# Performance work log

Hardware: AMD Instinct MI355X
Metric: run time of the kernel (lower is better)

## Reference

```python
import jax, jax.numpy as jnp
import numpy as np

N_QUBITS = 13
DEPTH = 4
DIM = 2 ** N_QUBITS
PI = 3.141592653589793

# qubit 0 = most significant bit of the basis-state index
_idx = np.arange(DIM)
BITS = np.stack([(_idx >> (N_QUBITS - 1 - q)) & 1 for q in range(N_QUBITS)], axis=1)  # (DIM, n)
SIGNS = jnp.asarray(1.0 - 2.0 * BITS, dtype=jnp.float32)                               # Z eigenvalues, (DIM, n)
PARITY = jnp.asarray((-1.0) ** BITS.sum(axis=1), dtype=jnp.float32)                    # <Z^{(x)n}> diagonal, (DIM,)
# CZ entangling chain (q, q+1): diagonal (-1)^{sum_q b_q b_{q+1}}
ENT = jnp.asarray((-1.0) ** (BITS[:, :-1] * BITS[:, 1:]).sum(axis=1), dtype=jnp.float32)


def fwht(psi):
    """Normalized fast Walsh-Hadamard transform (H on every qubit), psi: (B, DIM) complex."""
    B = psi.shape[0]
    for q in range(N_QUBITS):
        psi = psi.reshape(B, 2 ** q, 2, -1)
        psi = jnp.stack([psi[:, :, 0] + psi[:, :, 1], psi[:, :, 0] - psi[:, :, 1]], axis=2)
    return psi.reshape(B, DIM) * (2.0 ** (-N_QUBITS / 2))


def feature_map_state(x):
    """Havlicek ZZ feature map: psi = D(x) H^n D(x) H^n |0...0>.
    Diagonal phase per basis state b: sum_j x_j s_j(b) + sum_{j<k} (pi-x_j)(pi-x_k) s_j(b) s_k(b)."""
    a = PI - x                                              # (B, n)
    u = x @ SIGNS.T                                         # (B, DIM)
    v = a @ SIGNS.T                                         # (B, DIM)
    phi = u + 0.5 * (v * v - jnp.sum(a * a, axis=1, keepdims=True))  # pair term via (sum)^2 trick
    d = jnp.exp(1j * phi)                                   # complex64 diagonal
    psi = jnp.full((x.shape[0], DIM), DIM ** -0.5, dtype=jnp.complex64)  # H^n |0>
    psi = fwht(d * psi)
    return d * psi


def _apply_1q(psi, U, q):
    """Apply 2x2 complex gate U to qubit q (bit-sliced)."""
    B = psi.shape[0]
    psi = psi.reshape(B, 2 ** q, 2, -1)
    a0, a1 = psi[:, :, 0], psi[:, :, 1]
    out = jnp.stack([U[0, 0] * a0 + U[0, 1] * a1, U[1, 0] * a0 + U[1, 1] * a1], axis=2)
    return out.reshape(B, DIM)


def variational_apply(psi, theta):
    """(DEPTH+1) layers of per-qubit Rz(b)Ry(a), CZ-chain entanglers between layers."""
    th = theta.reshape(DEPTH + 1, N_QUBITS, 2)
    for l in range(DEPTH + 1):
        if l > 0:
            psi = psi * ENT
        for q in range(N_QUBITS):
            ca = jnp.cos(0.5 * th[l, q, 0])
            sa = jnp.sin(0.5 * th[l, q, 0])
            em = jnp.exp(-0.5j * th[l, q, 1])
            ep = jnp.exp(0.5j * th[l, q, 1])
            U = jnp.stack([jnp.stack([em * ca, -em * sa]), jnp.stack([ep * sa, ep * ca])])
            psi = _apply_1q(psi, U, q)
    return psi


def setup_inputs() -> dict:
    key = jax.random.key(0)
    k1, k2 = jax.random.split(key)
    x = jax.random.normal(k1, (512, N_QUBITS), dtype=jnp.float32)
    theta = 0.1 * jax.random.normal(k2, ((DEPTH + 1) * N_QUBITS * 2,), dtype=jnp.float32)
    bias = jnp.zeros((1,), dtype=jnp.float32)
    return {"x": x, "theta": theta, "bias": bias}


def reference(x, theta, bias):
    psi = feature_map_state(x)
    psi = variational_apply(psi, theta)
    prob = psi.real ** 2 + psi.imag ** 2              # (B, DIM)
    logit = prob @ PARITY + bias[0]                   # (B,)
    return jnp.stack([-logit, logit], axis=1)         # two-class logits
```

## Files before the change

### kernel.cpp

```cpp
#include <hip/hip_runtime.h>

#define NQ   13
#define DIM  8192
#define PI_F 3.14159265358979323846f
#define NT   256
#define NAMP 32

__device__ __forceinline__ int lslot(int i) { return i + (i >> 5); }
#define NSLOT (DIM + (DIM >> 5))

__device__ __forceinline__ void rsincos(float x, float* s, float* c) {
  const float INV2PI = 0.15915494309189535f;
  const float TWOPI  = 6.283185307179586f;
  float r = x * INV2PI;
  r -= rintf(r);
  float ang = r * TWOPI;
  *s = __sinf(ang);
  *c = __cosf(ang);
}

__device__ __forceinline__ void waveFence() {
  __builtin_amdgcn_wave_barrier();
  __threadfence_block();
  __builtin_amdgcn_wave_barrier();
}

__device__ __forceinline__ float2 f2fma(float s, float2 a, float2 b) {
  return make_float2(fmaf(s, a.x, b.x), fmaf(s, a.y, b.y));
}
__device__ __forceinline__ float2 f2add(float2 a, float2 b) {
  return make_float2(a.x + b.x, a.y + b.y);
}
__device__ __forceinline__ float2 f2sub(float2 a, float2 b) {
  return make_float2(a.x - b.x, a.y - b.y);
}
__device__ __forceinline__ float2 cphase(float2 v, float cs, float sn) {
  return make_float2(fmaf(cs, v.x, -sn * v.y), fmaf(cs, v.y, sn * v.x));
}
__device__ __forceinline__ float2 cmul(float2 a, float2 b) {
  return make_float2(fmaf(a.x, b.x, -a.y * b.y), fmaf(a.x, b.y, a.y * b.x));
}

template<int PAT>
__device__ __forceinline__ int ampIndex(int t, int j) {
  if constexpr (PAT == 0) return (t << 5) | j;
  else if constexpr (PAT == 1) return ((t >> 5) << 10) | (j << 5) | (t & 31);
  else return ((j >> 2) << 10) | (t << 2) | (j & 3);
}

template<int PAT>
__device__ __forceinline__ void buildTree(const float* __restrict__ w, float bias,
                                          int t, float* s) {
  float base = bias;
  if constexpr (PAT == 0) {
    #pragma unroll
    for (int k = 0; k < 8; k++) base += ((t >> k) & 1) ? w[5 + k] : 0.0f;
  } else if constexpr (PAT == 1) {
    #pragma unroll
    for (int k = 0; k < 5; k++) base += ((t >> k) & 1) ? w[k] : 0.0f;
    #pragma unroll
    for (int k = 0; k < 3; k++) base += ((t >> (5 + k)) & 1) ? w[10 + k] : 0.0f;
  } else {
    #pragma unroll
    for (int k = 0; k < 8; k++) base += ((t >> k) & 1) ? w[2 + k] : 0.0f;
  }
  constexpr int P[5] = { (PAT == 1) ? 5 : 0,
                         (PAT == 1) ? 6 : 1,
                         (PAT == 0) ? 2 : ((PAT == 1) ? 7 : 10),
                         (PAT == 0) ? 3 : ((PAT == 1) ? 8 : 11),
                         (PAT == 0) ? 4 : ((PAT == 1) ? 9 : 12) };
  s[0] = base;
  #pragma unroll
  for (int k = 0; k < 5; k++) {
    float wp = w[P[k]];
    #pragma unroll
    for (int m = 0; m < (1 << k); m++) s[m | (1 << k)] = s[m] + wp;
  }
}

template<int PAT>
__device__ __forceinline__ void loadAmps(const float2* __restrict__ sAmp,
                                         int t, float2* amp) {
  #pragma unroll
  for (int j = 0; j < NAMP; j++) {
    amp[j] = sAmp[lslot(ampIndex<PAT>(t, j))];
  }
}

template<int PAT>
__device__ __forceinline__ void storeAmps(float2* __restrict__ sAmp,
                                          int t, const float2* amp) {
  #pragma unroll
  for (int j = 0; j < NAMP; j++) {
    sAmp[lslot(ampIndex<PAT>(t, j))] = amp[j];
  }
}

template<int KB>
__device__ __forceinline__ void fwht_bit(float2* amp) {
  #pragma unroll
  for (int j = 0; j < NAMP; j++) if (!(j & (1 << KB))) {
    int j1 = j | (1 << KB);
    float2 a0 = amp[j], a1 = amp[j1];
    amp[j]  = f2add(a0, a1);
    amp[j1] = f2sub(a0, a1);
  }
}
__device__ __forceinline__ void fwht_all5(float2* amp) {
  fwht_bit<0>(amp); fwht_bit<1>(amp); fwht_bit<2>(amp);
  fwht_bit<3>(amp); fwht_bit<4>(amp);
}

template<int KB>
__device__ __forceinline__ void applyRy(float2* amp, float ta, float sa) {
  #pragma unroll
  for (int j = 0; j < NAMP; j++) if (!(j & (1 << KB))) {
    int j1 = j | (1 << KB);
    amp[j]  = f2fma(-ta, amp[j1], amp[j]);
    amp[j1] = f2fma( sa, amp[j],  amp[j1]);
    amp[j]  = f2fma(-ta, amp[j1], amp[j]);
  }
}

template<int PAT, bool INIT>
__device__ __forceinline__ void featureDiag(float2* amp,
                                            const float* __restrict__ wX,
                                            const float* __restrict__ wA,
                                            const float* __restrict__ cons, int t) {
  float u[NAMP], v[NAMP];
  buildTree<PAT>(wX, cons[0], t, u);
  buildTree<PAT>(wA, cons[1], t, v);
  float A2 = cons[2];
  #pragma unroll
  for (int j = 0; j < NAMP; j++) {
    float phi = u[j] + 0.5f * (v[j] * v[j] - A2);
    float sn, cs; rsincos(phi, &sn, &cs);
    if constexpr (INIT) amp[j] = make_float2(cs, sn);
    else                amp[j] = cphase(amp[j], cs, sn);
  }
}

__device__ __forceinline__ void applyDiagPT(float2* amp,
                                            const float* __restrict__ wb,
                                            const float* __restrict__ eR,
                                            const float* __restrict__ eI,
                                            float bias, int t) {
  float base = bias;
  #pragma unroll
  for (int k = 0; k < 8; k++) base += ((t >> k) & 1) ? wb[5 + k] : 0.0f;
  float2 c[NAMP];
  { float sn, cs; rsincos(base, &sn, &cs); c[0] = make_float2(cs, sn); }
  #pragma unroll
  for (int k = 0; k < 5; k++) {
    float2 e = make_float2(eR[k], eI[k]);
    #pragma unroll
    for (int m = 0; m < (1 << k); m++) c[m | (1 << k)] = cmul(c[m], e);
  }
  #pragma unroll
  for (int j = 0; j < NAMP; j++) {
    int i = ampIndex<0>(t, j);
    float sgn = (__popc(i & (i >> 1)) & 1) ? -1.0f : 1.0f;
    amp[j] = cphase(amp[j], c[j].x * sgn, c[j].y * sgn);
  }
}

__global__ __launch_bounds__(NT, 2) void qc_kernel(
    const float* __restrict__ xin,
    const float* __restrict__ thin,
    const float* __restrict__ bin,
    float* __restrict__ out) {
  __shared__ float2 sAmp[NSLOT];
  __shared__ float gTA[65], gSA[65];
  __shared__ float gBbit[65];
  __shared__ float eBr[65], eBi[65];
  __shared__ float wX[13], wA[13];
  __shared__ float cons[8];
  __shared__ float red[NT / 64];

  const int t = threadIdx.x;
  const int b = blockIdx.x;

  if (t < NQ) {
    float xq = xin[b * NQ + t];
    float aq = PI_F - xq;
    wX[12 - t] = -2.0f * xq;
    wA[12 - t] = -2.0f * aq;
  }
  if (t < 65) {
    float av = thin[2 * t];
    float bv = thin[2 * t + 1];
    float ca = cosf(0.5f * av);
    float sa = sinf(0.5f * av);
    gSA[t] = sa;
    gTA[t] = sa / (1.0f + ca);
    int l = t / NQ, q = t % NQ;
    int s = l * NQ + (12 - q);
    gBbit[s] = bv;
    eBr[s] = cosf(bv);
    eBi[s] = sinf(bv);
  }
  __syncthreads();
  if (t == 0) {
    float X = 0.f, A = 0.f, A2 = 0.f;
    for (int p = 0; p < NQ; p++) {
      float xq = -0.5f * wX[p], aq = -0.5f * wA[p];
      X += xq; A += aq; A2 += aq * aq;
    }
    cons[0] = X; cons[1] = A; cons[2] = A2;
    for (int l = 0; l < 5; l++) {
      float s = 0.f;
      for (int p = 0; p < NQ; p++) s += gBbit[l * NQ + p];
      cons[3 + l] = -0.5f * s;
    }
  }
  __syncthreads();

  float2 amp[NAMP];

  featureDiag<0, true>(amp, wX, wA, cons, t);
  fwht_all5(amp);
  storeAmps<0>(sAmp, t, amp);
  waveFence();

  loadAmps<1>(sAmp, t, amp);
  fwht_all5(amp);
  storeAmps<1>(sAmp, t, amp);
  __syncthreads();

  loadAmps<2>(sAmp, t, amp);
  fwht_bit<2>(amp); fwht_bit<3>(amp); fwht_bit<4>(amp);
  featureDiag<2, false>(amp, wX, wA, cons, t);
  storeAmps<2>(sAmp, t, amp);
  __syncthreads();

  float acc = 0.0f;
  for (int l = 0; l < 5; l++) {
    const int g = l * NQ;
    loadAmps<0>(sAmp, t, amp);
    if (l > 0) applyDiagPT(amp, gBbit + (l - 1) * NQ, eBr + (l - 1) * NQ,
                           eBi + (l - 1) * NQ, cons[3 + (l - 1)], t);
    applyRy<0>(amp, gTA[g + 12], gSA[g + 12]);
    applyRy<1>(amp, gTA[g + 11], gSA[g + 11]);
    applyRy<2>(amp, gTA[g + 10], gSA[g + 10]);
    applyRy<3>(amp, gTA[g + 9],  gSA[g + 9]);
    applyRy<4>(amp, gTA[g + 8],  gSA[g + 8]);
    storeAmps<0>(sAmp, t, amp);
    waveFence();
    loadAmps<1>(sAmp, t, amp);
    applyRy<0>(amp, gTA[g + 7], gSA[g + 7]);
    applyRy<1>(amp, gTA[g + 6], gSA[g + 6]);
    applyRy<2>(amp, gTA[g + 5], gSA[g + 5]);
    applyRy<3>(amp, gTA[g + 4], gSA[g + 4]);
    applyRy<4>(amp, gTA[g + 3], gSA[g + 3]);
    storeAmps<1>(sAmp, t, amp);
    __syncthreads();
    loadAmps<2>(sAmp, t, amp);
    applyRy<2>(amp, gTA[g + 2], gSA[g + 2]);
    applyRy<3>(amp, gTA[g + 1], gSA[g + 1]);
    applyRy<4>(amp, gTA[g + 0], gSA[g + 0]);
    if (l < 4) {
      storeAmps<2>(sAmp, t, amp);
      __syncthreads();
    } else {
      #pragma unroll
      for (int j = 0; j < NAMP; j++) {
        int i = ampIndex<2>(t, j);
        float p2 = fmaf(amp[j].x, amp[j].x, amp[j].y * amp[j].y);
        acc += (__popc(i) & 1) ? -p2 : p2;
      }
    }
  }

  #pragma unroll
  for (int off = 32; off > 0; off >>= 1) acc += __shfl_down(acc, off, 64);
  if ((t & 63) == 0) red[t >> 6] = acc;
  __syncthreads();
  if (t == 0) {
    float total = red[0] + red[1] + red[2] + red[3];
    float logit = total * (1.0f / 67108864.0f) + bin[0];
    out[b * 2 + 0] = -logit;
    out[b * 2 + 1] = logit;
  }
}

extern "C" void kernel_launch(void* const* d_in, const int* in_sizes, int n_in,
                              void* d_out, int out_size, void* d_ws, size_t ws_size,
                              hipStream_t stream) {
  const float* x  = (const float*)d_in[0];
  const float* th = (const float*)d_in[1];
  const float* bi = (const float*)d_in[2];
  float* out = (float*)d_out;
  int B = in_sizes[0] / NQ;
  qc_kernel<<<B, NT, 0, stream>>>(x, th, bi, out);
}
```

Before: 95.77 us.

## Regroup qubit passes into three stages and vectorize LDS amplitude access

Changes the LDS padding to two float2 per 32 amplitudes so pattern-0 and pattern-2 loads and stores can use float4 vector accesses. Reassigns qubits to passes: the pattern-2 pass now handles qubits 0,1,2,11,12 together with the entangling diagonal. This removes one LDS round trip and one __syncthreads per layer, and the last layer finishes in the pattern-1 pass. The goal is fewer LDS instructions and fewer block barriers, at the cost of a more intricate index mapping that could cause bank conflicts or correctness errors.

```diff
diff --git a/kernel.cpp b/kernel.cpp
--- a/kernel.cpp
+++ b/kernel.cpp
@@ -6,8 +6,8 @@
 #define NT   256
 #define NAMP 32
 
-__device__ __forceinline__ int lslot(int i) { return i + (i >> 5); }
-#define NSLOT (DIM + (DIM >> 5))
+__device__ __forceinline__ int lslot(int i) { return i + 2 * (i >> 5); }
+#define NSLOT (DIM + 2 * (DIM >> 5))
 
 __device__ __forceinline__ void rsincos(float x, float* s, float* c) {
   const float INV2PI = 0.15915494309189535f;
@@ -55,20 +55,14 @@
   if constexpr (PAT == 0) {
     #pragma unroll
     for (int k = 0; k < 8; k++) base += ((t >> k) & 1) ? w[5 + k] : 0.0f;
-  } else if constexpr (PAT == 1) {
-    #pragma unroll
-    for (int k = 0; k < 5; k++) base += ((t >> k) & 1) ? w[k] : 0.0f;
-    #pragma unroll
-    for (int k = 0; k < 3; k++) base += ((t >> (5 + k)) & 1) ? w[10 + k] : 0.0f;
   } else {
     #pragma unroll
     for (int k = 0; k < 8; k++) base += ((t >> k) & 1) ? w[2 + k] : 0.0f;
   }
-  constexpr int P[5] = { (PAT == 1) ? 5 : 0,
-                         (PAT == 1) ? 6 : 1,
-                         (PAT == 0) ? 2 : ((PAT == 1) ? 7 : 10),
-                         (PAT == 0) ? 3 : ((PAT == 1) ? 8 : 11),
-                         (PAT == 0) ? 4 : ((PAT == 1) ? 9 : 12) };
+  constexpr int P[5] = { 0, 1,
+                         (PAT == 0) ? 2 : 10,
+                         (PAT == 0) ? 3 : 11,
+                         (PAT == 0) ? 4 : 12 };
   s[0] = base;
   #pragma unroll
   for (int k = 0; k < 5; k++) {
@@ -78,21 +72,56 @@
   }
 }
 
-template<int PAT>
-__device__ __forceinline__ void loadAmps(const float2* __restrict__ sAmp,
-                                         int t, float2* amp) {
-  #pragma unroll
-  for (int j = 0; j < NAMP; j++) {
-    amp[j] = sAmp[lslot(ampIndex<PAT>(t, j))];
-  }
-}
-
-template<int PAT>
-__device__ __forceinline__ void storeAmps(float2* __restrict__ sAmp,
-                                          int t, const float2* amp) {
-  #pragma unroll
-  for (int j = 0; j < NAMP; j++) {
-    sAmp[lslot(ampIndex<PAT>(t, j))] = amp[j];
+__device__ __forceinline__ void loadAmps0(const float2* __restrict__ sAmp,
+                                          int t, float2* amp) {
+  const float4* p = reinterpret_cast<const float4*>(sAmp + 34 * t);
+  #pragma unroll
+  for (int k = 0; k < 16; k++) {
+    float4 v = p[k];
+    amp[2 * k]     = make_float2(v.x, v.y);
+    amp[2 * k + 1] = make_float2(v.z, v.w);
+  }
+}
+__device__ __forceinline__ void storeAmps0(float2* __restrict__ sAmp,
+                                           int t, const float2* amp) {
+  float4* p = reinterpret_cast<float4*>(sAmp + 34 * t);
+  #pragma unroll
+  for (int k = 0; k < 16; k++)
+    p[k] = make_float4(amp[2 * k].x, amp[2 * k].y, amp[2 * k + 1].x, amp[2 * k + 1].y);
+}
+
+__device__ __forceinline__ void loadAmps1(const float2* __restrict__ sAmp,
+                                          int t, float2* amp) {
+  #pragma unroll
+  for (int j = 0; j < NAMP; j++) amp[j] = sAmp[lslot(ampIndex<1>(t, j))];
+}
+__device__ __forceinline__ void storeAmps1(float2* __restrict__ sAmp,
+                                           int t, const float2* amp) {
+  #pragma unroll
+  for (int j = 0; j < NAMP; j++) sAmp[lslot(ampIndex<1>(t, j))] = amp[j];
+}
+
+__device__ __forceinline__ void loadAmps2(const float2* __restrict__ sAmp,
+                                          int t, float2* amp) {
+  int base = 4 * t + 2 * (t >> 3);
+  #pragma unroll
+  for (int g = 0; g < 8; g++) {
+    const float4* p = reinterpret_cast<const float4*>(sAmp + base + g * 1088);
+    float4 v0 = p[0], v1 = p[1];
+    amp[4 * g + 0] = make_float2(v0.x, v0.y);
+    amp[4 * g + 1] = make_float2(v0.z, v0.w);
+    amp[4 * g + 2] = make_float2(v1.x, v1.y);
+    amp[4 * g + 3] = make_float2(v1.z, v1.w);
+  }
+}
+__device__ __forceinline__ void storeAmps2(float2* __restrict__ sAmp,
+                                           int t, const float2* amp) {
+  int base = 4 * t + 2 * (t >> 3);
+  #pragma unroll
+  for (int g = 0; g < 8; g++) {
+    float4* p = reinterpret_cast<float4*>(sAmp + base + g * 1088);
+    p[0] = make_float4(amp[4 * g + 0].x, amp[4 * g + 0].y, amp[4 * g + 1].x, amp[4 * g + 1].y);
+    p[1] = make_float4(amp[4 * g + 2].x, amp[4 * g + 2].y, amp[4 * g + 3].x, amp[4 * g + 3].y);
   }
 }
 
@@ -140,25 +169,26 @@
   }
 }
 
-__device__ __forceinline__ void applyDiagPT(float2* amp,
-                                            const float* __restrict__ wb,
-                                            const float* __restrict__ eR,
-                                            const float* __restrict__ eI,
-                                            float bias, int t) {
+__device__ __forceinline__ void applyDiagPT2(float2* amp,
+                                             const float* __restrict__ wb,
+                                             const float* __restrict__ eR,
+                                             const float* __restrict__ eI,
+                                             float bias, int t) {
   float base = bias;
   #pragma unroll
-  for (int k = 0; k < 8; k++) base += ((t >> k) & 1) ? wb[5 + k] : 0.0f;
+  for (int k = 0; k < 8; k++) base += ((t >> k) & 1) ? wb[2 + k] : 0.0f;
   float2 c[NAMP];
   { float sn, cs; rsincos(base, &sn, &cs); c[0] = make_float2(cs, sn); }
+  constexpr int EB[5] = {0, 1, 10, 11, 12};
   #pragma unroll
   for (int k = 0; k < 5; k++) {
-    float2 e = make_float2(eR[k], eI[k]);
+    float2 e = make_float2(eR[EB[k]], eI[EB[k]]);
     #pragma unroll
     for (int m = 0; m < (1 << k); m++) c[m | (1 << k)] = cmul(c[m], e);
   }
   #pragma unroll
   for (int j = 0; j < NAMP; j++) {
-    int i = ampIndex<0>(t, j);
+    int i = ampIndex<2>(t, j);
     float sgn = (__popc(i & (i >> 1)) & 1) ? -1.0f : 1.0f;
     amp[j] = cphase(amp[j], c[j].x * sgn, c[j].y * sgn);
   }
@@ -219,55 +249,60 @@
 
   featureDiag<0, true>(amp, wX, wA, cons, t);
   fwht_all5(amp);
-  storeAmps<0>(sAmp, t, amp);
+  storeAmps0(sAmp, t, amp);
   waveFence();
 
-  loadAmps<1>(sAmp, t, amp);
+  loadAmps1(sAmp, t, amp);
   fwht_all5(amp);
-  storeAmps<1>(sAmp, t, amp);
-  __syncthreads();
-
-  loadAmps<2>(sAmp, t, amp);
+  storeAmps1(sAmp, t, amp);
+  __syncthreads();
+
+  loadAmps2(sAmp, t, amp);
   fwht_bit<2>(amp); fwht_bit<3>(amp); fwht_bit<4>(amp);
   featureDiag<2, false>(amp, wX, wA, cons, t);
-  storeAmps<2>(sAmp, t, amp);
+  applyRy<0>(amp, gTA[12], gSA[12]);
+  applyRy<1>(amp, gTA[11], gSA[11]);
+  applyRy<2>(amp, gTA[2],  gSA[2]);
+  applyRy<3>(amp, gTA[1],  gSA[1]);
+  applyRy<4>(amp, gTA[0],  gSA[0]);
+  storeAmps2(sAmp, t, amp);
   __syncthreads();
 
   float acc = 0.0f;
   for (int l = 0; l < 5; l++) {
     const int g = l * NQ;
-    loadAmps<0>(sAmp, t, amp);
-    if (l > 0) applyDiagPT(amp, gBbit + (l - 1) * NQ, eBr + (l - 1) * NQ,
-                           eBi + (l - 1) * NQ, cons[3 + (l - 1)], t);
-    applyRy<0>(amp, gTA[g + 12], gSA[g + 12]);
-    applyRy<1>(amp, gTA[g + 11], gSA[g + 11]);
+    loadAmps0(sAmp, t, amp);
     applyRy<2>(amp, gTA[g + 10], gSA[g + 10]);
     applyRy<3>(amp, gTA[g + 9],  gSA[g + 9]);
     applyRy<4>(amp, gTA[g + 8],  gSA[g + 8]);
-    storeAmps<0>(sAmp, t, amp);
+    storeAmps0(sAmp, t, amp);
     waveFence();
-    loadAmps<1>(sAmp, t, amp);
+    loadAmps1(sAmp, t, amp);
     applyRy<0>(amp, gTA[g + 7], gSA[g + 7]);
     applyRy<1>(amp, gTA[g + 6], gSA[g + 6]);
     applyRy<2>(amp, gTA[g + 5], gSA[g + 5]);
     applyRy<3>(amp, gTA[g + 4], gSA[g + 4]);
     applyRy<4>(amp, gTA[g + 3], gSA[g + 3]);
-    storeAmps<1>(sAmp, t, amp);
-    __syncthreads();
-    loadAmps<2>(sAmp, t, amp);
-    applyRy<2>(amp, gTA[g + 2], gSA[g + 2]);
-    applyRy<3>(amp, gTA[g + 1], gSA[g + 1]);
-    applyRy<4>(amp, gTA[g + 0], gSA[g + 0]);
-    if (l < 4) {
-      storeAmps<2>(sAmp, t, amp);
-      __syncthreads();
-    } else {
+    if (l == 4) {
       #pragma unroll
       for (int j = 0; j < NAMP; j++) {
-        int i = ampIndex<2>(t, j);
+        int i = ampIndex<1>(t, j);
         float p2 = fmaf(amp[j].x, amp[j].x, amp[j].y * amp[j].y);
         acc += (__popc(i) & 1) ? -p2 : p2;
       }
+    } else {
+      storeAmps1(sAmp, t, amp);
+      __syncthreads();
+      const int g1 = (l + 1) * NQ;
+      loadAmps2(sAmp, t, amp);
+      applyDiagPT2(amp, gBbit + l * NQ, eBr + l * NQ, eBi + l * NQ, cons[3 + l], t);
+      applyRy<0>(amp, gTA[g1 + 12], gSA[g1 + 12]);
+      applyRy<1>(amp, gTA[g1 + 11], gSA[g1 + 11]);
+      applyRy<2>(amp, gTA[g1 + 2],  gSA[g1 + 2]);
+      applyRy<3>(amp, gTA[g1 + 1],  gSA[g1 + 1]);
+      applyRy<4>(amp, gTA[g1 + 0],  gSA[g1 + 0]);
+      storeAmps2(sAmp, t, amp);
+      __syncthreads();
     }
   }
 
```

Result: slower. 120.9 us (+26.2%).
